# Performance work log

Hardware: AMD Instinct MI355X
Metric: run time of the kernel (lower is better)

Reference implementation:

```python
import jax, jax.numpy as jnp
import numpy as np

N_NODES = 50000
N_EDGES = 800000
NUM_FEAT = 100
F_DIM = 64
R_ROUNDS = 4
L_FP = 128
NUM_CLASS = 10


def setup_inputs() -> dict:
    key = jax.random.key(0)
    ks = jax.random.split(key, 10)
    s = 0.05
    return {
        "node_feature": jax.random.randint(ks[0], (N_NODES,), 0, NUM_FEAT),
        "edge_src": jax.random.randint(ks[1], (N_EDGES,), 0, N_NODES),
        "edge_dst": jax.random.randint(ks[2], (N_EDGES,), 0, N_NODES),
        "emb_table": jax.random.normal(ks[3], (NUM_FEAT, F_DIM), jnp.float32) * s,
        "W_h": jax.random.normal(ks[4], (R_ROUNDS, F_DIM, F_DIM), jnp.float32) * s,
        "b_h": jax.random.normal(ks[5], (R_ROUNDS, F_DIM), jnp.float32) * s,
        "W_fp": jax.random.normal(ks[6], (R_ROUNDS, F_DIM, L_FP), jnp.float32) * s,
        "b_fp": jax.random.normal(ks[7], (R_ROUNDS, L_FP), jnp.float32) * s,
        "W_cl": jax.random.normal(ks[8], (L_FP, NUM_CLASS), jnp.float32) * s,
        "b_cl": jax.random.normal(ks[9], (NUM_CLASS,), jnp.float32) * s,
    }


def reference(node_feature, edge_src, edge_dst, emb_table, W_h, b_h, W_fp, b_fp, W_cl, b_cl):
    # Initial node embeddings: [N, F]
    emb = emb_table[node_feature]
    f = jnp.zeros((L_FP,), dtype=emb.dtype)
    for r_i in range(R_ROUNDS):
        # v[node] = emb[node] + sum_{nbr in neighbours(node)} emb[nbr]
        agg = jax.ops.segment_sum(emb[edge_src], edge_dst, num_segments=N_NODES)
        v = emb + agg
        # per-node tiny MLP, batched over all nodes
        r = jax.nn.relu(v @ W_h[r_i] + b_h[r_i])            # [N, F]
        i = jax.nn.softmax(r @ W_fp[r_i] + b_fp[r_i], axis=-1)  # [N, L]
        f = f + i.sum(axis=0)                                # accumulate fingerprint
        emb = r                                              # synchronous update
    return jax.nn.softmax(f @ W_cl + b_cl, axis=-1)
```

## Files before the change

kernel.cpp:

```cpp
#include <hip/hip_runtime.h>
#include <hip/hip_bf16.h>

#define FDIM 64
#define LFP 128
#define RROUNDS 4
#define BM 64
#define PCHUNK 4096
#define CB 512
#define MAXB 10240
#define RSL 32

typedef __attribute__((ext_vector_type(8))) short bf16x8;
typedef __attribute__((ext_vector_type(4))) float f32x4;

__device__ __forceinline__ float bf2f(unsigned short u) {
    unsigned int x = ((unsigned int)u) << 16;
    float f;
    __builtin_memcpy(&f, &x, 4);
    return f;
}
__device__ __forceinline__ unsigned short f2bf(float x) {
    unsigned int u;
    __builtin_memcpy(&u, &x, 4);
    unsigned int r = (u + 0x7fffu + ((u >> 16) & 1u)) >> 16;
    return (unsigned short)r;
}

__global__ void setup_kernel(const int* __restrict__ feat, const float* __restrict__ table,
                             const float* __restrict__ Wh, const float* __restrict__ Wfp,
                             unsigned short* __restrict__ emb, unsigned short* __restrict__ whT,
                             unsigned short* __restrict__ wfpT, int* __restrict__ bucketCount,
                             int n) {
    int gid = blockIdx.x * blockDim.x + threadIdx.x;
    if (gid < RROUNDS * FDIM * FDIM) {
        int r = gid >> 12, rem = gid & 4095, j = rem >> 6, k = rem & 63;
        whT[gid] = f2bf(Wh[r * 4096 + k * 64 + j]);
    } else if (gid < RROUNDS * FDIM * FDIM + RROUNDS * LFP * FDIM) {
        int o2 = gid - RROUNDS * FDIM * FDIM;
        int r = o2 >> 13, rem = o2 & 8191, l = rem >> 6, k = rem & 63;
        wfpT[o2] = f2bf(Wfp[r * 8192 + k * 128 + l]);
    }
    if (gid < n * FDIM)
        emb[gid] = f2bf(table[feat[gid >> 6] * FDIM + (gid & 63)]);
    if (gid < 128) bucketCount[gid] = 0;
}

__global__ __launch_bounds__(256) void partition_kernel(
        const int* __restrict__ esrc, const int* __restrict__ edst,
        int* __restrict__ bucketCount, int* __restrict__ tmp, int nE, int nbc) {
    __shared__ int scnt[128], sinc[128], sexc[128], sgbase[128], scur[128];
    __shared__ int sbuf[PCHUNK];
    __shared__ int starg[PCHUNK];
    int t = threadIdx.x;
    int c0 = blockIdx.x * PCHUNK;
    int cend = c0 + PCHUNK; if (cend > nE) cend = nE;

    if (t < 128) scnt[t] = 0;
    __syncthreads();
#pragma unroll
    for (int k = 0; k < PCHUNK / 256; ++k) {
        int idx = c0 + k * 256 + t;
        if (idx < cend) atomicAdd(&scnt[edst[idx] >> 9], 1);
    }
    __syncthreads();
    if (t < 128) sinc[t] = scnt[t];
    __syncthreads();
    for (int d = 1; d < 128; d <<= 1) {
        int x = (t >= d && t < 128) ? sinc[t - d] : 0;
        __syncthreads();
        if (t < 128) sinc[t] += x;
        __syncthreads();
    }
    if (t < 128) {
        int ex = sinc[t] - scnt[t];
        sexc[t] = ex;
        scur[t] = ex;
        sgbase[t] = (t < nbc && scnt[t] > 0)
                        ? t * MAXB + atomicAdd(&bucketCount[t], scnt[t]) : 0;
    }
    __syncthreads();
#pragma unroll
    for (int k = 0; k < PCHUNK / 256; ++k) {
        int idx = c0 + k * 256 + t;
        if (idx < cend) {
            int s = esrc[idx], d = edst[idx];
            int b = d >> 9;
            int pos = atomicAdd(&scur[b], 1);
            sbuf[pos] = (s << 9) | (d & 511);
            starg[pos] = sgbase[b] + (pos - sexc[b]);
        }
    }
    __syncthreads();
    int cnt = cend - c0;
#pragma unroll
    for (int k = 0; k < PCHUNK / 256; ++k) {
        int li = k * 256 + t;
        if (li < cnt) tmp[starg[li]] = sbuf[li];
    }
}

__global__ __launch_bounds__(256) void bsort_kernel(
        const int* __restrict__ bucketCount, const int* __restrict__ tmp,
        unsigned short* __restrict__ csr16, int* __restrict__ rp, int N, int nE, int nbc) {
    __shared__ unsigned short ssrc[MAXB];
    __shared__ int pcnt[CB], pexc[CB], pcur[CB];
    __shared__ int ssum[256];
    __shared__ int sS[128];
    int t = threadIdx.x;
    int b = blockIdx.x;

    if (t < 128) sS[t] = (t < nbc) ? bucketCount[t] : 0;
    __syncthreads();
    for (int d = 1; d < 128; d <<= 1) {
        int x = (t >= d && t < 128) ? sS[t - d] : 0;
        __syncthreads();
        if (t < 128) sS[t] += x;
        __syncthreads();
    }
    int lo = (b == 0) ? 0 : sS[b - 1];
    int cnt = sS[b] - lo;

    pcnt[t] = 0; pcnt[t + 256] = 0;
    __syncthreads();
    const int* bt = tmp + (size_t)b * MAXB;
    for (int idx = t; idx < cnt; idx += 256)
        atomicAdd(&pcnt[bt[idx] & 511], 1);
    __syncthreads();
    int a0 = pcnt[2 * t], a1 = pcnt[2 * t + 1];
    ssum[t] = a0 + a1;
    __syncthreads();
    for (int d = 1; d < 256; d <<= 1) {
        int x = (t >= d) ? ssum[t - d] : 0;
        __syncthreads();
        ssum[t] += x;
        __syncthreads();
    }
    int ex = ssum[t] - (a0 + a1);
    pexc[2 * t] = ex;          pcur[2 * t] = ex;
    pexc[2 * t + 1] = ex + a0; pcur[2 * t + 1] = ex + a0;
    __syncthreads();
#pragma unroll
    for (int i = t; i < CB; i += 256) {
        int node = b * CB + i;
        if (node < N) rp[node] = lo + pexc[i];
    }
    if (b == 0 && t == 0) rp[N] = nE;
    for (int idx = t; idx < cnt; idx += 256) {
        int e = bt[idx];
        int pos = atomicAdd(&pcur[e & 511], 1);
        ssrc[pos] = (unsigned short)(e >> 9);
    }
    __syncthreads();
    for (int li = t; li < cnt; li += 256) csr16[lo + li] = ssrc[li];
}

__global__ __launch_bounds__(256) void round_kernel(
        const unsigned short* __restrict__ embIn, unsigned short* __restrict__ embOut,
        const int* __restrict__ rp, const unsigned short* __restrict__ csr16,
        const unsigned short* __restrict__ whT, const unsigned short* __restrict__ wfpT,
        const float* __restrict__ bh, const float* __restrict__ bfp,
        float* __restrict__ fpart, int N) {
    __shared__ unsigned short sV[BM * 72];
    __shared__ unsigned short sR[BM * 72];
    __shared__ float sFp[4][128];

    int tid = threadIdx.x;
    int base = blockIdx.x * BM;
    int lane = tid & 63, w = tid >> 6;
    int grp = lane >> 3, q = lane & 7;

    int nn = base + w * 16 + lane;
    if (nn > N) nn = N;
    int rpv = (lane < 17) ? rp[nn] : 0;

#pragma unroll
    for (int i = 0; i < 16; ++i) {
        int node = base + w * 16 + i;
        int start = __shfl(rpv, i);
        int end = __shfl(rpv, i + 1);
        if (node < N) {
            int last = end - 1;
            bf16x8 self = *reinterpret_cast<const bf16x8*>(embIn + (size_t)node * 64 + q * 8);
            float acc[8] = {0.f, 0.f, 0.f, 0.f, 0.f, 0.f, 0.f, 0.f};
            for (int j = start + grp; j < end; j += 32) {
                int j1 = j + 8, j2 = j + 16, j3 = j + 24;
                int c1 = j1 <= last ? j1 : last;
                int c2 = j2 <= last ? j2 : last;
                int c3 = j3 <= last ? j3 : last;
                int n0 = csr16[j];
                int n1 = csr16[c1];
                int n2 = csr16[c2];
                int n3 = csr16[c3];
                bf16x8 u0 = *reinterpret_cast<const bf16x8*>(embIn + (size_t)n0 * 64 + q * 8);
                bf16x8 u1 = *reinterpret_cast<const bf16x8*>(embIn + (size_t)n1 * 64 + q * 8);
                bf16x8 u2 = *reinterpret_cast<const bf16x8*>(embIn + (size_t)n2 * 64 + q * 8);
                bf16x8 u3 = *reinterpret_cast<const bf16x8*>(embIn + (size_t)n3 * 64 + q * 8);
                float m1 = (j1 <= last) ? 1.f : 0.f;
                float m2 = (j2 <= last) ? 1.f : 0.f;
                float m3 = (j3 <= last) ? 1.f : 0.f;
#pragma unroll
                for (int x = 0; x < 8; ++x) {
                    acc[x] += bf2f((unsigned short)u0[x]);
                    acc[x] = fmaf(m1, bf2f((unsigned short)u1[x]), acc[x]);
                    acc[x] = fmaf(m2, bf2f((unsigned short)u2[x]), acc[x]);
                    acc[x] = fmaf(m3, bf2f((unsigned short)u3[x]), acc[x]);
                }
            }
#pragma unroll
            for (int x = 0; x < 8; ++x) {
                acc[x] += __shfl_xor(acc[x], 8);
                acc[x] += __shfl_xor(acc[x], 16);
                acc[x] += __shfl_xor(acc[x], 32);
            }
            if (grp == 0) {
                bf16x8 o;
#pragma unroll
                for (int x = 0; x < 8; ++x) o[x] = (short)f2bf(acc[x] + bf2f((unsigned short)self[x]));
                *reinterpret_cast<bf16x8*>(sV + (w * 16 + i) * 72 + q * 8) = o;
            }
        } else if (grp == 0) {
            bf16x8 o;
#pragma unroll
            for (int x = 0; x < 8; ++x) o[x] = 0;
            *reinterpret_cast<bf16x8*>(sV + (w * 16 + i) * 72 + q * 8) = o;
        }
    }

    int m16 = lane & 15, g = lane >> 4;
    int arow = w * 16 + m16;

    bf16x8 a0 = *reinterpret_cast<const bf16x8*>(sV + arow * 72 + g * 8);
    bf16x8 a1 = *reinterpret_cast<const bf16x8*>(sV + arow * 72 + 32 + g * 8);

    f32x4 acc[4];
#pragma unroll
    for (int c = 0; c < 4; ++c) {
        bf16x8 b0 = *reinterpret_cast<const bf16x8*>(whT + (c * 16 + m16) * 64 + g * 8);
        bf16x8 b1 = *reinterpret_cast<const bf16x8*>(whT + (c * 16 + m16) * 64 + 32 + g * 8);
        f32x4 z = {0.f, 0.f, 0.f, 0.f};
        z = __builtin_amdgcn_mfma_f32_16x16x32_bf16(a0, b0, z, 0, 0, 0);
        z = __builtin_amdgcn_mfma_f32_16x16x32_bf16(a1, b1, z, 0, 0, 0);
        acc[c] = z;
    }
#pragma unroll
    for (int c = 0; c < 4; ++c) {
        float bias = bh[c * 16 + m16];
#pragma unroll
        for (int reg = 0; reg < 4; ++reg) {
            float rv = fmaxf(acc[c][reg] + bias, 0.f);
            sR[(w * 16 + g * 4 + reg) * 72 + c * 16 + m16] = f2bf(rv);
        }
    }

    bf16x8 ra0 = *reinterpret_cast<const bf16x8*>(sR + arow * 72 + g * 8);
    bf16x8 ra1 = *reinterpret_cast<const bf16x8*>(sR + arow * 72 + 32 + g * 8);

#pragma unroll
    for (int it = 0; it < 2; ++it) {
        int lidx = w * 1024 + it * 512 + lane * 8;
        int row = lidx >> 6;
        if (base + row < N)
            *reinterpret_cast<bf16x8*>(embOut + (size_t)base * 64 + lidx) =
                *reinterpret_cast<const bf16x8*>(sR + row * 72 + (lidx & 63));
    }

    f32x4 z[8];
#pragma unroll
    for (int t = 0; t < 8; ++t) {
        bf16x8 b0 = *reinterpret_cast<const bf16x8*>(wfpT + (t * 16 + m16) * 64 + g * 8);
        bf16x8 b1 = *reinterpret_cast<const bf16x8*>(wfpT + (t * 16 + m16) * 64 + 32 + g * 8);
        f32x4 zz = {0.f, 0.f, 0.f, 0.f};
        zz = __builtin_amdgcn_mfma_f32_16x16x32_bf16(ra0, b0, zz, 0, 0, 0);
        zz = __builtin_amdgcn_mfma_f32_16x16x32_bf16(ra1, b1, zz, 0, 0, 0);
        float bias = bfp[t * 16 + m16];
#pragma unroll
        for (int reg = 0; reg < 4; ++reg) zz[reg] += bias;
        z[t] = zz;
    }

#pragma unroll
    for (int reg = 0; reg < 4; ++reg) {
        float mx = -1e30f;
#pragma unroll
        for (int t = 0; t < 8; ++t) mx = fmaxf(mx, z[t][reg]);
#pragma unroll
        for (int d = 1; d < 16; d <<= 1) mx = fmaxf(mx, __shfl_xor(mx, d));
        float s = 0.f;
#pragma unroll
        for (int t = 0; t < 8; ++t) {
            float p = __expf(z[t][reg] - mx);
            z[t][reg] = p;
            s += p;
        }
#pragma unroll
        for (int d = 1; d < 16; d <<= 1) s += __shfl_xor(s, d);
        int node = base + w * 16 + g * 4 + reg;
        float inv = (node < N) ? (1.f / s) : 0.f;
#pragma unroll
        for (int t = 0; t < 8; ++t) z[t][reg] *= inv;
    }
#pragma unroll
    for (int t = 0; t < 8; ++t) {
        float v = z[t][0] + z[t][1] + z[t][2] + z[t][3];
        v += __shfl_xor(v, 16);
        v += __shfl_xor(v, 32);
        if (g == 0) sFp[w][t * 16 + m16] = v;
    }
    __syncthreads();
    if (tid < 128) {
        float s = sFp[0][tid] + sFp[1][tid] + sFp[2][tid] + sFp[3][tid];
        fpart[(size_t)blockIdx.x * 128 + tid] = s;
    }
}

__global__ __launch_bounds__(256) void reduce1_kernel(const float* __restrict__ fpart,
                                                      float* __restrict__ fred, int nslice) {
    __shared__ float sAcc[128];
    int t = threadIdx.x;
    int col = t & 127, gp = t >> 7;
    int base = blockIdx.x * RSL + gp * (RSL / 2);
    const float* p = fpart + (size_t)base * 128 + col;
    float a0 = 0.f, a1 = 0.f, a2 = 0.f, a3 = 0.f;
    if (base + RSL / 2 <= nslice) {
#pragma unroll
        for (int k = 0; k < 4; ++k) {
            a0 += p[(k * 4 + 0) * 128];
            a1 += p[(k * 4 + 1) * 128];
            a2 += p[(k * 4 + 2) * 128];
            a3 += p[(k * 4 + 3) * 128];
        }
    } else {
        int cnt = nslice - base; if (cnt < 0) cnt = 0;
        for (int k = 0; k < cnt; ++k) a0 += p[k * 128];
    }
    float s = (a0 + a1) + (a2 + a3);
    if (gp == 1) sAcc[col] = s;
    __syncthreads();
    if (gp == 0) fred[(size_t)blockIdx.x * 128 + col] = s + sAcc[col];
}

__global__ __launch_bounds__(256) void final_kernel(const float* __restrict__ fred, int nred,
                                                    const float* __restrict__ Wcl,
                                                    const float* __restrict__ bcl,
                                                    float* __restrict__ out) {
    __shared__ float sAcc[128];
    __shared__ float sf[128];
    __shared__ float logits[10];
    int t = threadIdx.x;
    int col = t & 127, gp = t >> 7;
    int half = (nred + 1) >> 1;
    int b0 = gp * half;
    int b1 = b0 + half; if (b1 > nred) b1 = nred;
    float a0 = 0.f, a1 = 0.f, a2 = 0.f, a3 = 0.f;
    const float* p = fred + col;
    int b = b0;
    for (; b + 4 <= b1; b += 4) {
        a0 += p[(size_t)(b + 0) * 128];
        a1 += p[(size_t)(b + 1) * 128];
        a2 += p[(size_t)(b + 2) * 128];
        a3 += p[(size_t)(b + 3) * 128];
    }
    for (; b < b1; ++b) a0 += p[(size_t)b * 128];
    float s = (a0 + a1) + (a2 + a3);
    if (gp == 1) sAcc[col] = s;
    __syncthreads();
    if (gp == 0) sf[col] = s + sAcc[col];
    __syncthreads();
    if (t < 10) {
        float acc = bcl[t];
        for (int l = 0; l < LFP; l++) acc = fmaf(sf[l], Wcl[l * 10 + t], acc);
        logits[t] = acc;
    }
    __syncthreads();
    if (t == 0) {
        float m = -1e30f;
        for (int i = 0; i < 10; i++) m = fmaxf(m, logits[i]);
        float e[10], s2 = 0.f;
        for (int i = 0; i < 10; i++) { e[i] = __expf(logits[i] - m); s2 += e[i]; }
        for (int i = 0; i < 10; i++) out[i] = e[i] / s2;
    }
}

extern "C" void kernel_launch(void* const* d_in, const int* in_sizes, int n_in,
                              void* d_out, int out_size, void* d_ws, size_t ws_size,
                              hipStream_t stream) {
    const int* feat = (const int*)d_in[0];
    const int* esrc = (const int*)d_in[1];
    const int* edst = (const int*)d_in[2];
    const float* table = (const float*)d_in[3];
    const float* Wh = (const float*)d_in[4];
    const float* bh = (const float*)d_in[5];
    const float* Wfp = (const float*)d_in[6];
    const float* bfp = (const float*)d_in[7];
    const float* Wcl = (const float*)d_in[8];
    const float* bcl = (const float*)d_in[9];
    float* out = (float*)d_out;
    int N = in_sizes[0];
    int nE = in_sizes[1];

    int nbm = (N + BM - 1) / BM;
    int nbc = (N + CB - 1) / CB;
    int nbp = (nE + PCHUNK - 1) / PCHUNK;
    int nslice = RROUNDS * nbm;
    int nred = (nslice + RSL - 1) / RSL;

    char* ws = (char*)d_ws;
    size_t off = 0;
    auto alloc = [&](size_t bytes) { void* p = ws + off; off += (bytes + 63) & ~(size_t)63; return p; };
    unsigned short* embA = (unsigned short*)alloc((size_t)N * 64 * 2);
    unsigned short* embB = (unsigned short*)alloc((size_t)N * 64 * 2);
    unsigned short* whT  = (unsigned short*)alloc(RROUNDS * 64 * 64 * 2);
    unsigned short* wfpT = (unsigned short*)alloc(RROUNDS * 128 * 64 * 2);
    float* fpart = (float*)alloc((size_t)nslice * 128 * 4);
    float* fred  = (float*)alloc((size_t)nred * 128 * 4);
    int* bucketCount = (int*)alloc(128 * 4);
    int* rp      = (int*)alloc(((size_t)N + 1) * 4);
    int* tmp     = (int*)alloc((size_t)nbc * MAXB * 4);
    unsigned short* csr16 = (unsigned short*)alloc((size_t)nE * 2);

    setup_kernel<<<(N * FDIM + 255) / 256, 256, 0, stream>>>(
        feat, table, Wh, Wfp, embA, whT, wfpT, bucketCount, N);

    partition_kernel<<<nbp, 256, 0, stream>>>(esrc, edst, bucketCount, tmp, nE, nbc);
    bsort_kernel<<<nbc, 256, 0, stream>>>(bucketCount, tmp, csr16, rp, N, nE, nbc);

    unsigned short* eIn = embA;
    unsigned short* eOut = embB;
    for (int r = 0; r < RROUNDS; ++r) {
        round_kernel<<<nbm, 256, 0, stream>>>(
            eIn, eOut, rp, csr16, whT + (size_t)r * 4096, wfpT + (size_t)r * 8192,
            bh + (size_t)r * FDIM, bfp + (size_t)r * LFP,
            fpart + (size_t)r * nbm * 128, N);
        unsigned short* t = eIn; eIn = eOut; eOut = t;
    }

    reduce1_kernel<<<nred, 256, 0, stream>>>(fpart, fred, nslice);
    final_kernel<<<1, 256, 0, stream>>>(fred, nred, Wcl, bcl, out);
}
```

Before: 210.1 us.

## Fuse setup with partition and reduce with final via last-block completion

Merges the embedding/weight setup kernel with the edge partition kernel into one launch, and merges the two-stage fingerprint reduction with the final classifier using an atomic last-block-done counter. The partition no longer uses global atomics on bucket counters. Each chunk instead writes per-chunk bucket counts and offsets, and the bucket sort kernel scans these and binary-searches to gather its edges. The aim is to remove two kernel launches and the global atomic contention, at the cost of extra scans and binary searches per edge in bsort and a grid-wide fence/atomic in the reduction.

Measured after the change: 243.1 us. 15.7% more time.

```diff
diff --git a/kernel.cpp b/kernel.cpp
--- a/kernel.cpp
+++ b/kernel.cpp
@@ -26,105 +26,119 @@
     return (unsigned short)r;
 }
 
-__global__ void setup_kernel(const int* __restrict__ feat, const float* __restrict__ table,
-                             const float* __restrict__ Wh, const float* __restrict__ Wfp,
-                             unsigned short* __restrict__ emb, unsigned short* __restrict__ whT,
-                             unsigned short* __restrict__ wfpT, int* __restrict__ bucketCount,
-                             int n) {
-    int gid = blockIdx.x * blockDim.x + threadIdx.x;
-    if (gid < RROUNDS * FDIM * FDIM) {
-        int r = gid >> 12, rem = gid & 4095, j = rem >> 6, k = rem & 63;
-        whT[gid] = f2bf(Wh[r * 4096 + k * 64 + j]);
-    } else if (gid < RROUNDS * FDIM * FDIM + RROUNDS * LFP * FDIM) {
-        int o2 = gid - RROUNDS * FDIM * FDIM;
-        int r = o2 >> 13, rem = o2 & 8191, l = rem >> 6, k = rem & 63;
-        wfpT[o2] = f2bf(Wfp[r * 8192 + k * 128 + l]);
-    }
-    if (gid < n * FDIM)
-        emb[gid] = f2bf(table[feat[gid >> 6] * FDIM + (gid & 63)]);
-    if (gid < 128) bucketCount[gid] = 0;
-}
-
-__global__ __launch_bounds__(256) void partition_kernel(
+__global__ __launch_bounds__(256) void setup_partition_kernel(
+        const int* __restrict__ feat, const float* __restrict__ table,
+        const float* __restrict__ Wh, const float* __restrict__ Wfp,
+        unsigned short* __restrict__ emb, unsigned short* __restrict__ whT,
+        unsigned short* __restrict__ wfpT,
         const int* __restrict__ esrc, const int* __restrict__ edst,
-        int* __restrict__ bucketCount, int* __restrict__ tmp, int nE, int nbc) {
-    __shared__ int scnt[128], sinc[128], sexc[128], sgbase[128], scur[128];
+        int* __restrict__ pcnts, int* __restrict__ pexcg, int* __restrict__ tmp,
+        int* __restrict__ done, int n, int nE, int nbp) {
+    __shared__ int scnt[128], sinc[128], scur[128];
     __shared__ int sbuf[PCHUNK];
-    __shared__ int starg[PCHUNK];
+    int b = blockIdx.x;
     int t = threadIdx.x;
-    int c0 = blockIdx.x * PCHUNK;
-    int cend = c0 + PCHUNK; if (cend > nE) cend = nE;
-
-    if (t < 128) scnt[t] = 0;
-    __syncthreads();
-#pragma unroll
-    for (int k = 0; k < PCHUNK / 256; ++k) {
-        int idx = c0 + k * 256 + t;
-        if (idx < cend) atomicAdd(&scnt[edst[idx] >> 9], 1);
-    }
-    __syncthreads();
-    if (t < 128) sinc[t] = scnt[t];
-    __syncthreads();
-    for (int d = 1; d < 128; d <<= 1) {
-        int x = (t >= d && t < 128) ? sinc[t - d] : 0;
-        __syncthreads();
-        if (t < 128) sinc[t] += x;
-        __syncthreads();
-    }
-    if (t < 128) {
-        int ex = sinc[t] - scnt[t];
-        sexc[t] = ex;
-        scur[t] = ex;
-        sgbase[t] = (t < nbc && scnt[t] > 0)
-                        ? t * MAXB + atomicAdd(&bucketCount[t], scnt[t]) : 0;
-    }
-    __syncthreads();
-#pragma unroll
-    for (int k = 0; k < PCHUNK / 256; ++k) {
-        int idx = c0 + k * 256 + t;
-        if (idx < cend) {
-            int s = esrc[idx], d = edst[idx];
-            int b = d >> 9;
-            int pos = atomicAdd(&scur[b], 1);
-            sbuf[pos] = (s << 9) | (d & 511);
-            starg[pos] = sgbase[b] + (pos - sexc[b]);
-        }
-    }
-    __syncthreads();
-    int cnt = cend - c0;
-#pragma unroll
-    for (int k = 0; k < PCHUNK / 256; ++k) {
-        int li = k * 256 + t;
-        if (li < cnt) tmp[starg[li]] = sbuf[li];
+    if (b < nbp) {
+        int c0 = b * PCHUNK;
+        int cend = c0 + PCHUNK; if (cend > nE) cend = nE;
+        if (t < 128) scnt[t] = 0;
+        __syncthreads();
+#pragma unroll
+        for (int k = 0; k < PCHUNK / 256; ++k) {
+            int idx = c0 + k * 256 + t;
+            if (idx < cend) atomicAdd(&scnt[edst[idx] >> 9], 1);
+        }
+        __syncthreads();
+        if (t < 128) sinc[t] = scnt[t];
+        __syncthreads();
+        for (int d = 1; d < 128; d <<= 1) {
+            int x = (t >= d && t < 128) ? sinc[t - d] : 0;
+            __syncthreads();
+            if (t < 128) sinc[t] += x;
+            __syncthreads();
+        }
+        if (t < 128) {
+            int ex = sinc[t] - scnt[t];
+            scur[t] = ex;
+            pcnts[b * 128 + t] = scnt[t];
+            pexcg[b * 128 + t] = ex;
+        }
+        __syncthreads();
+#pragma unroll
+        for (int k = 0; k < PCHUNK / 256; ++k) {
+            int idx = c0 + k * 256 + t;
+            if (idx < cend) {
+                int s = esrc[idx], d = edst[idx];
+                int pos = atomicAdd(&scur[d >> 9], 1);
+                sbuf[pos] = (s << 9) | (d & 511);
+            }
+        }
+        __syncthreads();
+        int cnt = cend - c0;
+#pragma unroll
+        for (int k = 0; k < PCHUNK / 256; ++k) {
+            int li = k * 256 + t;
+            if (li < cnt) tmp[c0 + li] = sbuf[li];
+        }
+    } else {
+        int gid = (b - nbp) * 256 + t;
+        if (gid < RROUNDS * FDIM * FDIM) {
+            int r = gid >> 12, rem = gid & 4095, j = rem >> 6, k = rem & 63;
+            whT[gid] = f2bf(Wh[r * 4096 + k * 64 + j]);
+        } else if (gid < RROUNDS * FDIM * FDIM + RROUNDS * LFP * FDIM) {
+            int o2 = gid - RROUNDS * FDIM * FDIM;
+            int r = o2 >> 13, rem = o2 & 8191, l = rem >> 6, k = rem & 63;
+            wfpT[o2] = f2bf(Wfp[r * 8192 + k * 128 + l]);
+        }
+        if (gid < n * FDIM)
+            emb[gid] = f2bf(table[feat[gid >> 6] * FDIM + (gid & 63)]);
+        if (gid == 0) *done = 0;
     }
 }
 
 __global__ __launch_bounds__(256) void bsort_kernel(
-        const int* __restrict__ bucketCount, const int* __restrict__ tmp,
-        unsigned short* __restrict__ csr16, int* __restrict__ rp, int N, int nE, int nbc) {
-    __shared__ unsigned short ssrc[MAXB];
+        const int* __restrict__ pcnts, const int* __restrict__ pexcg,
+        const int* __restrict__ tmp, unsigned short* __restrict__ csr16,
+        int* __restrict__ rp, int N, int nE, int nbp) {
+    __shared__ int rIncl[256], rExcl[256], rBase[256];
     __shared__ int pcnt[CB], pexc[CB], pcur[CB];
     __shared__ int ssum[256];
-    __shared__ int sS[128];
+    __shared__ unsigned short ssrc[MAXB];
+    __shared__ int sTot, sLo;
     int t = threadIdx.x;
-    int b = blockIdx.x;
-
-    if (t < 128) sS[t] = (t < nbc) ? bucketCount[t] : 0;
-    __syncthreads();
-    for (int d = 1; d < 128; d <<= 1) {
-        int x = (t >= d && t < 128) ? sS[t - d] : 0;
-        __syncthreads();
-        if (t < 128) sS[t] += x;
-        __syncthreads();
-    }
-    int lo = (b == 0) ? 0 : sS[b - 1];
-    int cnt = sS[b] - lo;
-
+    int c = blockIdx.x;
+
+    int v = (t < nbp) ? pcnts[t * 128 + c] : 0;
+    int pe = (t < nbp) ? pexcg[t * 128 + c] : 0;
+    rBase[t] = t * PCHUNK + pe;
+    rIncl[t] = v;
+    __syncthreads();
+    for (int d = 1; d < 256; d <<= 1) {
+        int x = (t >= d) ? rIncl[t - d] : 0;
+        __syncthreads();
+        rIncl[t] += x;
+        __syncthreads();
+    }
+    rExcl[t] = rIncl[t] - v;
+    ssum[t] = pe;
+    __syncthreads();
+    for (int d = 1; d < 256; d <<= 1) {
+        int x = (t >= d) ? ssum[t - d] : 0;
+        __syncthreads();
+        ssum[t] += x;
+        __syncthreads();
+    }
+    if (t == 255) { sTot = rIncl[255]; sLo = ssum[255]; }
     pcnt[t] = 0; pcnt[t + 256] = 0;
     __syncthreads();
-    const int* bt = tmp + (size_t)b * MAXB;
-    for (int idx = t; idx < cnt; idx += 256)
-        atomicAdd(&pcnt[bt[idx] & 511], 1);
+    int cnt = sTot, lo = sLo;
+
+    for (int g = t; g < cnt; g += 256) {
+        int loB = 0, hiB = nbp - 1;
+        while (loB < hiB) { int mid = (loB + hiB) >> 1; if (g < rIncl[mid]) hiB = mid; else loB = mid + 1; }
+        int e = tmp[rBase[loB] + (g - rExcl[loB])];
+        atomicAdd(&pcnt[e & 511], 1);
+    }
     __syncthreads();
     int a0 = pcnt[2 * t], a1 = pcnt[2 * t + 1];
     ssum[t] = a0 + a1;
@@ -141,12 +155,14 @@
     __syncthreads();
 #pragma unroll
     for (int i = t; i < CB; i += 256) {
-        int node = b * CB + i;
+        int node = c * CB + i;
         if (node < N) rp[node] = lo + pexc[i];
     }
-    if (b == 0 && t == 0) rp[N] = nE;
-    for (int idx = t; idx < cnt; idx += 256) {
-        int e = bt[idx];
+    if (c == 0 && t == 0) rp[N] = nE;
+    for (int g = t; g < cnt; g += 256) {
+        int loB = 0, hiB = nbp - 1;
+        while (loB < hiB) { int mid = (loB + hiB) >> 1; if (g < rIncl[mid]) hiB = mid; else loB = mid + 1; }
+        int e = tmp[rBase[loB] + (g - rExcl[loB])];
         int pos = atomicAdd(&pcur[e & 511], 1);
         ssrc[pos] = (unsigned short)(e >> 9);
     }
@@ -313,41 +329,46 @@
     }
 }
 
-__global__ __launch_bounds__(256) void reduce1_kernel(const float* __restrict__ fpart,
-                                                      float* __restrict__ fred, int nslice) {
-    __shared__ float sAcc[128];
-    int t = threadIdx.x;
-    int col = t & 127, gp = t >> 7;
-    int base = blockIdx.x * RSL + gp * (RSL / 2);
-    const float* p = fpart + (size_t)base * 128 + col;
-    float a0 = 0.f, a1 = 0.f, a2 = 0.f, a3 = 0.f;
-    if (base + RSL / 2 <= nslice) {
-#pragma unroll
-        for (int k = 0; k < 4; ++k) {
-            a0 += p[(k * 4 + 0) * 128];
-            a1 += p[(k * 4 + 1) * 128];
-            a2 += p[(k * 4 + 2) * 128];
-            a3 += p[(k * 4 + 3) * 128];
-        }
-    } else {
-        int cnt = nslice - base; if (cnt < 0) cnt = 0;
-        for (int k = 0; k < cnt; ++k) a0 += p[k * 128];
-    }
-    float s = (a0 + a1) + (a2 + a3);
-    if (gp == 1) sAcc[col] = s;
-    __syncthreads();
-    if (gp == 0) fred[(size_t)blockIdx.x * 128 + col] = s + sAcc[col];
-}
-
-__global__ __launch_bounds__(256) void final_kernel(const float* __restrict__ fred, int nred,
-                                                    const float* __restrict__ Wcl,
-                                                    const float* __restrict__ bcl,
-                                                    float* __restrict__ out) {
+__global__ __launch_bounds__(256) void reduce_final_kernel(
+        const float* __restrict__ fpart, float* __restrict__ fred, int nslice,
+        const float* __restrict__ Wcl, const float* __restrict__ bcl,
+        float* __restrict__ out, int* __restrict__ done) {
     __shared__ float sAcc[128];
     __shared__ float sf[128];
     __shared__ float logits[10];
+    __shared__ int lastFlag;
     int t = threadIdx.x;
     int col = t & 127, gp = t >> 7;
+    {
+        int base = blockIdx.x * RSL + gp * (RSL / 2);
+        const float* p = fpart + (size_t)base * 128 + col;
+        float a0 = 0.f, a1 = 0.f, a2 = 0.f, a3 = 0.f;
+        if (base + RSL / 2 <= nslice) {
+#pragma unroll
+            for (int k = 0; k < 4; ++k) {
+                a0 += p[(k * 4 + 0) * 128];
+                a1 += p[(k * 4 + 1) * 128];
+                a2 += p[(k * 4 + 2) * 128];
+                a3 += p[(k * 4 + 3) * 128];
+            }
+        } else {
+            int cnt = nslice - base; if (cnt < 0) cnt = 0;
+            for (int k = 0; k < cnt; ++k) a0 += p[k * 128];
+        }
+        float s = (a0 + a1) + (a2 + a3);
+        if (gp == 1) sAcc[col] = s;
+        __syncthreads();
+        if (gp == 0) fred[(size_t)blockIdx.x * 128 + col] = s + sAcc[col];
+    }
+    __threadfence();
+    __syncthreads();
+    if (t == 0)
+        lastFlag = (__hip_atomic_fetch_add(done, 1, __ATOMIC_ACQ_REL, __HIP_MEMORY_SCOPE_AGENT)
+                    == (int)gridDim.x - 1);
+    __syncthreads();
+    if (!lastFlag) return;
+
+    int nred = (int)gridDim.x;
     int half = (nred + 1) >> 1;
     int b0 = gp * half;
     int b1 = b0 + half; if (b1 > nred) b1 = nred;
@@ -362,6 +383,7 @@
     }
     for (; b < b1; ++b) a0 += p[(size_t)b * 128];
     float s = (a0 + a1) + (a2 + a3);
+    __syncthreads();
     if (gp == 1) sAcc[col] = s;
     __syncthreads();
     if (gp == 0) sf[col] = s + sAcc[col];
@@ -413,16 +435,19 @@
     unsigned short* wfpT = (unsigned short*)alloc(RROUNDS * 128 * 64 * 2);
     float* fpart = (float*)alloc((size_t)nslice * 128 * 4);
     float* fred  = (float*)alloc((size_t)nred * 128 * 4);
-    int* bucketCount = (int*)alloc(128 * 4);
+    int* pcnts   = (int*)alloc((size_t)nbp * 128 * 4);
+    int* pexcg   = (int*)alloc((size_t)nbp * 128 * 4);
+    int* done    = (int*)alloc(64);
     int* rp      = (int*)alloc(((size_t)N + 1) * 4);
-    int* tmp     = (int*)alloc((size_t)nbc * MAXB * 4);
+    int* tmp     = (int*)alloc((size_t)nbp * PCHUNK * 4);
     unsigned short* csr16 = (unsigned short*)alloc((size_t)nE * 2);
 
-    setup_kernel<<<(N * FDIM + 255) / 256, 256, 0, stream>>>(
-        feat, table, Wh, Wfp, embA, whT, wfpT, bucketCount, N);
-
-    partition_kernel<<<nbp, 256, 0, stream>>>(esrc, edst, bucketCount, tmp, nE, nbc);
-    bsort_kernel<<<nbc, 256, 0, stream>>>(bucketCount, tmp, csr16, rp, N, nE, nbc);
+    int setupBlocks = (N * FDIM + 255) / 256;
+    setup_partition_kernel<<<nbp + setupBlocks, 256, 0, stream>>>(
+        feat, table, Wh, Wfp, embA, whT, wfpT, esrc, edst,
+        pcnts, pexcg, tmp, done, N, nE, nbp);
+
+    bsort_kernel<<<nbc, 256, 0, stream>>>(pcnts, pexcg, tmp, csr16, rp, N, nE, nbp);
 
     unsigned short* eIn = embA;
     unsigned short* eOut = embB;
@@ -434,6 +459,5 @@
         unsigned short* t = eIn; eIn = eOut; eOut = t;
     }
 
-    reduce1_kernel<<<nred, 256, 0, stream>>>(fpart, fred, nslice);
-    final_kernel<<<1, 256, 0, stream>>>(fred, nred, Wcl, bcl, out);
-}
+    reduce_final_kernel<<<nred, 256, 0, stream>>>(fpart, fred, nslice, Wcl, bcl, out, done);
+}
```
